# Kernel tuning notes

Measured on AMD Instinct MI355X. Metric: run time of the kernel, lower is better.

The kernel has to match this reference:

```python
import jax, jax.numpy as jnp
import numpy as np

N = 100000      # nodes
E = 1600000     # directed edges (avg degree 16)
IN, HID, OUT = 128, 128, 64


def setup_inputs() -> dict:
    key = jax.random.key(0)
    ks = jax.random.split(key, 6)
    x = jax.random.normal(ks[0], (N, IN), dtype=jnp.float32)
    edge_index = jax.random.randint(ks[1], (2, E), 0, N, dtype=jnp.int32)
    W1 = jax.random.normal(ks[2], (IN, HID), dtype=jnp.float32) * (1.0 / np.sqrt(IN))
    b1 = jax.random.normal(ks[3], (HID,), dtype=jnp.float32) * 0.01
    W2 = jax.random.normal(ks[4], (HID, OUT), dtype=jnp.float32) * (1.0 / np.sqrt(HID))
    b2 = jax.random.normal(ks[5], (OUT,), dtype=jnp.float32) * 0.01
    return {"x": x, "edge_index": edge_index, "W1": W1, "b1": b1, "W2": W2, "b2": b2}


def _gcn_norm(edge_index):
    # add self-loops, compute symmetric normalization deg^-1/2 A_hat deg^-1/2
    loop = jnp.arange(N, dtype=edge_index.dtype)
    row = jnp.concatenate([edge_index[0], loop])  # source
    col = jnp.concatenate([edge_index[1], loop])  # target
    deg = jax.ops.segment_sum(jnp.ones(row.shape[0], jnp.float32), col, num_segments=N)
    dinv = jnp.where(deg > 0, jax.lax.rsqrt(deg), 0.0)
    norm = dinv[row] * dinv[col]  # [E+N]
    return row, col, norm


def _gcn_conv(x, row, col, norm, W, b):
    h = x @ W                              # [N, out] dense transform first (fewer features moved)
    msg = h[row] * norm[:, None]           # gather over edges
    agg = jax.ops.segment_sum(msg, col, num_segments=N)  # scatter-add to targets
    return agg + b


def reference(x, edge_index, W1, b1, W2, b2):
    row, col, norm = _gcn_norm(edge_index)
    h = jax.nn.relu(_gcn_conv(x, row, col, norm, W1, b1))
    return _gcn_conv(h, row, col, norm, W2, b2)
```

## Files before the change

### kernel.cpp

```cpp
#include <hip/hip_runtime.h>

#define NN 100000
#define NE 1600000

#define BSH 9
#define BSZ 512
#define NBUK 196
#define CAP 12288
#define CHUNK 4096
#define EPT 16

typedef _Float16 hs8 __attribute__((ext_vector_type(8)));
typedef float f32x4 __attribute__((ext_vector_type(4)));
typedef float f32x2 __attribute__((ext_vector_type(2)));
#define MFMA16H(a, b, c) __builtin_amdgcn_mfma_f32_16x16x32_f16(a, b, c, 0, 0, 0)

static inline size_t alignup(size_t x) { return (x + 255) & ~(size_t)255; }

union h8u { uint4 q; _Float16 h[8]; };


__global__ __launch_bounds__(256) void k_prep0(int* __restrict__ gcur,
                                               const float* __restrict__ W1, _Float16* __restrict__ WT1,
                                               const float* __restrict__ W2, _Float16* __restrict__ WT2) {
  int b = blockIdx.x, t = threadIdx.x;
  if (b < 64) {
    int i = b * 256 + t;
    int k = i >> 7, c = i & 127;
    WT1[c * 128 + k] = (_Float16)W1[i];
  } else if (b < 96) {
    int i = (b - 64) * 256 + t;
    int k = i >> 6, c = i & 63;
    WT2[c * 128 + k] = (_Float16)W2[i];
  } else {
    if (t < NBUK) gcur[t] = t * CAP;
  }
}

__global__ __launch_bounds__(256) void k_bucket(const int* __restrict__ row, const int* __restrict__ col,
                                                int* __restrict__ gcur, uint* __restrict__ pr_pack) {
  __shared__ int cnt[NBUK];
  int t = threadIdx.x;
  for (int i = t; i < NBUK; i += 256) cnt[i] = 0;
  __syncthreads();
  int e0 = blockIdx.x * CHUNK;
  int rr[EPT], cc[EPT];
#pragma unroll
  for (int i = 0; i < EPT; i++) {
    int e = e0 + t + i * 256;
    bool ok = e < NE;
    cc[i] = ok ? col[e] : -1;
    rr[i] = ok ? row[e] : 0;
  }
#pragma unroll
  for (int i = 0; i < EPT; i++)
    if (cc[i] >= 0) atomicAdd(&cnt[cc[i] >> BSH], 1);
  __syncthreads();
  for (int i = t; i < NBUK; i += 256) {
    int c = cnt[i];
    cnt[i] = c ? atomicAdd(&gcur[i], c) : 0;
  }
  __syncthreads();
#pragma unroll
  for (int i = 0; i < EPT; i++)
    if (cc[i] >= 0) {
      int p = atomicAdd(&cnt[cc[i] >> BSH], 1);
      pr_pack[p] = ((uint)rr[i] << BSH) | (uint)(cc[i] & (BSZ - 1));
    }
}

__global__ __launch_bounds__(256) void k_bdeg(const uint* __restrict__ pr_pack, const int* __restrict__ gcur,
                                              int* __restrict__ deg, float* __restrict__ dinv,
                                              int* __restrict__ bsums) {
  __shared__ int dc[BSZ];
  int t = threadIdx.x, b = blockIdx.x;
  for (int i = t; i < BSZ; i += 256) dc[i] = 0;
  __syncthreads();
  int s = b * CAP;
  int n = min(gcur[b] - s, CAP);
  for (int i = t; i < n; i += 256) atomicAdd(&dc[pr_pack[s + i] & (BSZ - 1)], 1);
  __syncthreads();
  int nb0 = b << BSH;
  for (int i = t; i < BSZ; i += 256) {
    int node = nb0 + i;
    if (node < NN) {
      int d = dc[i] + 1;
      deg[node] = d;
      dinv[node] = rsqrtf((float)d);
    }
  }
  if (t == 0) bsums[b] = n + min(BSZ, NN - nb0);
}

__global__ __launch_bounds__(256) void k_scanB(int* __restrict__ bsums) {
  __shared__ int sm[256];
  int t = threadIdx.x;
  int v = (t < NBUK) ? bsums[t] : 0;
  sm[t] = v;
  __syncthreads();
  for (int d = 1; d < 256; d <<= 1) {
    int tmp = (t >= d) ? sm[t - d] : 0;
    __syncthreads();
    sm[t] += tmp;
    __syncthreads();
  }
  if (t < NBUK) bsums[t] = sm[t] - v;
}

__global__ __launch_bounds__(256) void k_bfill(const uint* __restrict__ pr_pack, const int* __restrict__ gcur,
                                               const int* __restrict__ deg, const float* __restrict__ dinv,
                                               const int* __restrict__ bsums, int* __restrict__ offs,
                                               uint2* __restrict__ wcsr) {
  __shared__ int loff[BSZ];
  __shared__ int cur[BSZ];
  __shared__ float dl[BSZ];
  __shared__ int tsum[256];
  int t = threadIdx.x, b = blockIdx.x;
  int nb0 = b << BSH;
  int i0 = 2 * t, i1 = i0 + 1;
  int n0 = nb0 + i0, n1 = nb0 + i1;
  int d0 = (n0 < NN) ? deg[n0] : 0;
  int d1 = (n1 < NN) ? deg[n1] : 0;
  int v = d0 + d1;
  tsum[t] = v;
  __syncthreads();
  for (int d = 1; d < 256; d <<= 1) {
    int tmp = (t >= d) ? tsum[t - d] : 0;
    __syncthreads();
    tsum[t] += tmp;
    __syncthreads();
  }
  int base = bsums[b] + tsum[t] - v;
  float dv0 = (n0 < NN) ? dinv[n0] : 0.f;
  float dv1 = (n1 < NN) ? dinv[n1] : 0.f;
  loff[i0] = base;
  loff[i1] = base + d0;
  dl[i0] = dv0;
  dl[i1] = dv1;
  cur[i0] = 1;
  cur[i1] = 1;
  if (n0 < NN) {
    offs[n0] = base;
    wcsr[base] = make_uint2((uint)n0, __float_as_uint(dv0 * dv0));
  }
  if (n1 < NN) {
    offs[n1] = base + d0;
    wcsr[base + d0] = make_uint2((uint)n1, __float_as_uint(dv1 * dv1));
  }
  __syncthreads();
  int s = b * CAP;
  int n = min(gcur[b] - s, CAP);
  for (int i = t; i < n; i += 256) {
    uint prk = pr_pack[s + i];
    int li = (int)(prk & (BSZ - 1));
    uint r = prk >> BSH;
    int p = atomicAdd(&cur[li], 1);
    wcsr[loff[li] + p] = make_uint2(r, __float_as_uint(dinv[r] * dl[li]));
  }
}


__global__ __launch_bounds__(256) void k_gemm128(const float* __restrict__ x, const _Float16* __restrict__ WT,
                                                 unsigned char* __restrict__ t8) {
  int wave = threadIdx.x >> 6, lane = threadIdx.x & 63;
  int col0 = wave * 32;
  int lr = lane & 15;
  int lk = (lane >> 4) * 8;
  hs8 bfrag[2][4];
#pragma unroll
  for (int n = 0; n < 2; n++)
#pragma unroll
    for (int ks = 0; ks < 4; ks++)
      bfrag[n][ks] = *(const hs8*)&WT[(size_t)(col0 + n * 16 + lr) * 128 + ks * 32 + lk];
  int row0 = blockIdx.x * 64;
#pragma unroll 1
  for (int mt = 0; mt < 4; mt++) {
    int r0 = row0 + mt * 16;
    if (r0 >= NN) return;
    const float* xr = x + (size_t)(r0 + lr) * 128 + lk;
    f32x4 acc[2] = {{0.f, 0.f, 0.f, 0.f}, {0.f, 0.f, 0.f, 0.f}};
#pragma unroll
    for (int ks = 0; ks < 4; ks++) {
      float4 a0 = *(const float4*)&xr[ks * 32];
      float4 a1 = *(const float4*)&xr[ks * 32 + 4];
      hs8 af;
      af[0] = (_Float16)a0.x; af[1] = (_Float16)a0.y;
      af[2] = (_Float16)a0.z; af[3] = (_Float16)a0.w;
      af[4] = (_Float16)a1.x; af[5] = (_Float16)a1.y;
      af[6] = (_Float16)a1.z; af[7] = (_Float16)a1.w;
      acc[0] = MFMA16H(af, bfrag[0][ks], acc[0]);
      acc[1] = MFMA16H(af, bfrag[1][ks], acc[1]);
    }
    int rbase = r0 + (lane >> 4) * 4;
#pragma unroll
    for (int n = 0; n < 2; n++)
#pragma unroll
      for (int r = 0; r < 4; r++) {
        uint e = (uint)__builtin_amdgcn_cvt_pk_fp8_f32(acc[n][r], acc[n][r], 0, false);
        t8[(size_t)(rbase + r) * 128 + col0 + n * 16 + lr] = (unsigned char)(e & 0xffu);
      }
  }
}

__global__ __launch_bounds__(256) void k_gemm64(const _Float16* __restrict__ h, const _Float16* __restrict__ WT,
                                                _Float16* __restrict__ t2) {
  int wave = threadIdx.x >> 6, lane = threadIdx.x & 63;
  int col0 = wave * 16;
  int lr = lane & 15;
  int lk = (lane >> 4) * 8;
  hs8 bfrag[4];
#pragma unroll
  for (int ks = 0; ks < 4; ks++)
    bfrag[ks] = *(const hs8*)&WT[(size_t)(col0 + lr) * 128 + ks * 32 + lk];
  int row0 = blockIdx.x * 64;
#pragma unroll 1
  for (int mt = 0; mt < 4; mt++) {
    int r0 = row0 + mt * 16;
    if (r0 >= NN) return;
    const _Float16* hr = h + (size_t)(r0 + lr) * 128 + lk;
    f32x4 acc = {0.f, 0.f, 0.f, 0.f};
#pragma unroll
    for (int ks = 0; ks < 4; ks++) {
      hs8 af = *(const hs8*)&hr[ks * 32];
      acc = MFMA16H(af, bfrag[ks], acc);
    }
    int rbase = r0 + (lane >> 4) * 4;
#pragma unroll
    for (int r = 0; r < 4; r++)
      t2[(size_t)(rbase + r) * 64 + col0 + lr] = (_Float16)acc[r];
  }
}


__global__ __launch_bounds__(256) void k_agg128(const unsigned char* __restrict__ t8, const int* __restrict__ offs,
                                                const int* __restrict__ deg, const uint2* __restrict__ wcsr,
                                                const float* __restrict__ bias, _Float16* __restrict__ out) {
  int wave = threadIdx.x >> 6, lane = threadIdx.x & 63;
  int half = lane >> 5;
  int sub = (lane >> 4) & 1;
  int f = lane & 15;
  int node = blockIdx.x * 8 + wave * 2 + half;
  int beg = offs[node];
  int d = deg[node];
  const char* tb = (const char*)t8;
  float acc[8] = {};
  int trips = (d + 1) >> 1;
  uint2 e = (sub < d) ? wcsr[beg + sub] : make_uint2(0u, 0u);
#pragma unroll 1
  for (int k = 0; k < trips; k++) {
    int ns = (k + 1) * 2 + sub;
    uint2 en = (ns < d) ? wcsr[beg + ns] : make_uint2(0u, 0u);
    float s = __uint_as_float(e.y);
    uint2 u = *(const uint2*)(tb + (((size_t)e.x) << 7) + (f << 3));
    f32x2 p0 = __builtin_amdgcn_cvt_pk_f32_fp8(u.x, false);
    f32x2 p1 = __builtin_amdgcn_cvt_pk_f32_fp8(u.x, true);
    f32x2 p2 = __builtin_amdgcn_cvt_pk_f32_fp8(u.y, false);
    f32x2 p3 = __builtin_amdgcn_cvt_pk_f32_fp8(u.y, true);
    acc[0] = fmaf(p0[0], s, acc[0]);
    acc[1] = fmaf(p0[1], s, acc[1]);
    acc[2] = fmaf(p1[0], s, acc[2]);
    acc[3] = fmaf(p1[1], s, acc[3]);
    acc[4] = fmaf(p2[0], s, acc[4]);
    acc[5] = fmaf(p2[1], s, acc[5]);
    acc[6] = fmaf(p3[0], s, acc[6]);
    acc[7] = fmaf(p3[1], s, acc[7]);
    e = en;
  }
#pragma unroll
  for (int j = 0; j < 8; j++) acc[j] += __shfl_xor(acc[j], 16);
  if (sub == 0) {
    float4 b0 = *(const float4*)&bias[f * 8];
    float4 b1 = *(const float4*)&bias[f * 8 + 4];
    h8u st;
    st.h[0] = (_Float16)fmaxf(acc[0] + b0.x, 0.f);
    st.h[1] = (_Float16)fmaxf(acc[1] + b0.y, 0.f);
    st.h[2] = (_Float16)fmaxf(acc[2] + b0.z, 0.f);
    st.h[3] = (_Float16)fmaxf(acc[3] + b0.w, 0.f);
    st.h[4] = (_Float16)fmaxf(acc[4] + b1.x, 0.f);
    st.h[5] = (_Float16)fmaxf(acc[5] + b1.y, 0.f);
    st.h[6] = (_Float16)fmaxf(acc[6] + b1.z, 0.f);
    st.h[7] = (_Float16)fmaxf(acc[7] + b1.w, 0.f);
    *(uint4*)&out[(size_t)node * 128 + f * 8] = st.q;
  }
}

__global__ __launch_bounds__(256) void k_agg64(const _Float16* __restrict__ t, const int* __restrict__ offs,
                                               const int* __restrict__ deg, const uint2* __restrict__ wcsr,
                                               const float* __restrict__ bias, float* __restrict__ out) {
  int wave = threadIdx.x >> 6, lane = threadIdx.x & 63;
  int half = lane >> 5;
  int sub = (lane >> 3) & 3;
  int f8 = lane & 7;
  int node = blockIdx.x * 8 + wave * 2 + half;
  int beg = offs[node];
  int d = deg[node];
  const char* tb = (const char*)t;
  float acc[8] = {};
  int trips = (d + 3) >> 2;
  uint2 e = (sub < d) ? wcsr[beg + sub] : make_uint2(0u, 0u);
#pragma unroll 1
  for (int k = 0; k < trips; k++) {
    int ns = (k + 1) * 4 + sub;
    uint2 en = (ns < d) ? wcsr[beg + ns] : make_uint2(0u, 0u);
    float s = __uint_as_float(e.y);
    h8u u;
    u.q = *(const uint4*)(tb + (((size_t)e.x) << 7) + (f8 << 4));
    acc[0] = fmaf((float)u.h[0], s, acc[0]);
    acc[1] = fmaf((float)u.h[1], s, acc[1]);
    acc[2] = fmaf((float)u.h[2], s, acc[2]);
    acc[3] = fmaf((float)u.h[3], s, acc[3]);
    acc[4] = fmaf((float)u.h[4], s, acc[4]);
    acc[5] = fmaf((float)u.h[5], s, acc[5]);
    acc[6] = fmaf((float)u.h[6], s, acc[6]);
    acc[7] = fmaf((float)u.h[7], s, acc[7]);
    e = en;
  }
#pragma unroll
  for (int j = 0; j < 8; j++) {
    acc[j] += __shfl_xor(acc[j], 8);
    acc[j] += __shfl_xor(acc[j], 16);
  }
  if (sub == 0) {
    float4 b0 = *(const float4*)&bias[f8 * 8];
    float4 b1 = *(const float4*)&bias[f8 * 8 + 4];
    float4 o0 = make_float4(acc[0] + b0.x, acc[1] + b0.y, acc[2] + b0.z, acc[3] + b0.w);
    float4 o1 = make_float4(acc[4] + b1.x, acc[5] + b1.y, acc[6] + b1.z, acc[7] + b1.w);
    *(float4*)&out[(size_t)node * 64 + f8 * 8] = o0;
    *(float4*)&out[(size_t)node * 64 + f8 * 8 + 4] = o1;
  }
}


extern "C" void kernel_launch(void* const* d_in, const int* in_sizes, int n_in,
                              void* d_out, int out_size, void* d_ws, size_t ws_size,
                              hipStream_t stream) {
  const float* x  = (const float*)d_in[0];
  const int*   ei = (const int*)d_in[1];
  const float* W1 = (const float*)d_in[2];
  const float* b1 = (const float*)d_in[3];
  const float* W2 = (const float*)d_in[4];
  const float* b2 = (const float*)d_in[5];
  float* out = (float*)d_out;

  char* p = (char*)d_ws;
  int* deg       = (int*)p;      p += alignup((size_t)NN * 4);
  int* gcur      = (int*)p;      p += alignup((size_t)NBUK * 4);
  int* offs      = (int*)p;      p += alignup((size_t)NN * 4);
  int* bsums     = (int*)p;      p += alignup(256 * 4);
  float* dinv    = (float*)p;    p += alignup((size_t)NN * 4);
  uint2* wcsr    = (uint2*)p;    p += alignup((size_t)(NE + NN + 64) * 8);
  _Float16* WT1  = (_Float16*)p; p += alignup(128 * 128 * 2);
  _Float16* WT2  = (_Float16*)p; p += alignup(64 * 128 * 2);
  unsigned char* t8 = (unsigned char*)p; p += alignup((size_t)NN * 128);
  _Float16* t2   = (_Float16*)p; p += alignup((size_t)NN * 64 * 2);
  _Float16* h1   = (_Float16*)p; p += alignup((size_t)NN * 128 * 2);
  uint* pr_pack  = (uint*)t2;
  (void)ws_size; (void)in_sizes; (void)n_in; (void)out_size;

  const int* row = ei;
  const int* col = ei + NE;

  int nbB = (NE + CHUNK - 1) / CHUNK;

  k_prep0<<<97, 256, 0, stream>>>(gcur, W1, WT1, W2, WT2);
  k_bucket<<<nbB, 256, 0, stream>>>(row, col, gcur, pr_pack);
  k_bdeg<<<NBUK, 256, 0, stream>>>(pr_pack, gcur, deg, dinv, bsums);
  k_scanB<<<1, 256, 0, stream>>>(bsums);
  k_bfill<<<NBUK, 256, 0, stream>>>(pr_pack, gcur, deg, dinv, bsums, offs, wcsr);

  int nbG = (NN + 63) / 64;
  int nbA = NN / 8;
  k_gemm128<<<nbG, 256, 0, stream>>>(x, WT1, t8);
  k_agg128<<<nbA, 256, 0, stream>>>(t8, offs, deg, wcsr, b1, h1);
  k_gemm64<<<nbG, 256, 0, stream>>>(h1, WT2, t2);
  k_agg64<<<nbA, 256, 0, stream>>>(t2, offs, deg, wcsr, b2, out);
}
```

Baseline: 195.5 us.

## Fuse edge bucketing with first GEMM, drop scan kernel, software-pipeline aggregations

Edge bucketing and the first dense transform now run in one launch, with separate block ranges, so they can overlap on the device. The block-sum scan kernel is removed: each fill block reserves its CSR segment base with an atomic on a global counter. CSR segments therefore land in arbitrary block order, which is fine because aggregation reads them through offs and deg. Both aggregation kernels prefetch edge records two steps ahead and feature rows one step ahead to hide gather latency, and the 128-wide one uses packed two-wide FMAs. The cost is more live registers and one extra speculative gather per node.

```diff
diff --git a/kernel.cpp b/kernel.cpp
--- a/kernel.cpp
+++ b/kernel.cpp
@@ -20,7 +20,7 @@
 union h8u { uint4 q; _Float16 h[8]; };
 
 
-__global__ __launch_bounds__(256) void k_prep0(int* __restrict__ gcur,
+__global__ __launch_bounds__(256) void k_prep0(int* __restrict__ gcur, int* __restrict__ gtotal,
                                                const float* __restrict__ W1, _Float16* __restrict__ WT1,
                                                const float* __restrict__ W2, _Float16* __restrict__ WT2) {
   int b = blockIdx.x, t = threadIdx.x;
@@ -34,134 +34,13 @@
     WT2[c * 128 + k] = (_Float16)W2[i];
   } else {
     if (t < NBUK) gcur[t] = t * CAP;
-  }
-}
-
-__global__ __launch_bounds__(256) void k_bucket(const int* __restrict__ row, const int* __restrict__ col,
-                                                int* __restrict__ gcur, uint* __restrict__ pr_pack) {
-  __shared__ int cnt[NBUK];
-  int t = threadIdx.x;
-  for (int i = t; i < NBUK; i += 256) cnt[i] = 0;
-  __syncthreads();
-  int e0 = blockIdx.x * CHUNK;
-  int rr[EPT], cc[EPT];
-#pragma unroll
-  for (int i = 0; i < EPT; i++) {
-    int e = e0 + t + i * 256;
-    bool ok = e < NE;
-    cc[i] = ok ? col[e] : -1;
-    rr[i] = ok ? row[e] : 0;
-  }
-#pragma unroll
-  for (int i = 0; i < EPT; i++)
-    if (cc[i] >= 0) atomicAdd(&cnt[cc[i] >> BSH], 1);
-  __syncthreads();
-  for (int i = t; i < NBUK; i += 256) {
-    int c = cnt[i];
-    cnt[i] = c ? atomicAdd(&gcur[i], c) : 0;
-  }
-  __syncthreads();
-#pragma unroll
-  for (int i = 0; i < EPT; i++)
-    if (cc[i] >= 0) {
-      int p = atomicAdd(&cnt[cc[i] >> BSH], 1);
-      pr_pack[p] = ((uint)rr[i] << BSH) | (uint)(cc[i] & (BSZ - 1));
-    }
-}
-
-__global__ __launch_bounds__(256) void k_bdeg(const uint* __restrict__ pr_pack, const int* __restrict__ gcur,
-                                              int* __restrict__ deg, float* __restrict__ dinv,
-                                              int* __restrict__ bsums) {
-  __shared__ int dc[BSZ];
-  int t = threadIdx.x, b = blockIdx.x;
-  for (int i = t; i < BSZ; i += 256) dc[i] = 0;
-  __syncthreads();
-  int s = b * CAP;
-  int n = min(gcur[b] - s, CAP);
-  for (int i = t; i < n; i += 256) atomicAdd(&dc[pr_pack[s + i] & (BSZ - 1)], 1);
-  __syncthreads();
-  int nb0 = b << BSH;
-  for (int i = t; i < BSZ; i += 256) {
-    int node = nb0 + i;
-    if (node < NN) {
-      int d = dc[i] + 1;
-      deg[node] = d;
-      dinv[node] = rsqrtf((float)d);
-    }
-  }
-  if (t == 0) bsums[b] = n + min(BSZ, NN - nb0);
-}
-
-__global__ __launch_bounds__(256) void k_scanB(int* __restrict__ bsums) {
-  __shared__ int sm[256];
-  int t = threadIdx.x;
-  int v = (t < NBUK) ? bsums[t] : 0;
-  sm[t] = v;
-  __syncthreads();
-  for (int d = 1; d < 256; d <<= 1) {
-    int tmp = (t >= d) ? sm[t - d] : 0;
-    __syncthreads();
-    sm[t] += tmp;
-    __syncthreads();
-  }
-  if (t < NBUK) bsums[t] = sm[t] - v;
-}
-
-__global__ __launch_bounds__(256) void k_bfill(const uint* __restrict__ pr_pack, const int* __restrict__ gcur,
-                                               const int* __restrict__ deg, const float* __restrict__ dinv,
-                                               const int* __restrict__ bsums, int* __restrict__ offs,
-                                               uint2* __restrict__ wcsr) {
-  __shared__ int loff[BSZ];
-  __shared__ int cur[BSZ];
-  __shared__ float dl[BSZ];
-  __shared__ int tsum[256];
-  int t = threadIdx.x, b = blockIdx.x;
-  int nb0 = b << BSH;
-  int i0 = 2 * t, i1 = i0 + 1;
-  int n0 = nb0 + i0, n1 = nb0 + i1;
-  int d0 = (n0 < NN) ? deg[n0] : 0;
-  int d1 = (n1 < NN) ? deg[n1] : 0;
-  int v = d0 + d1;
-  tsum[t] = v;
-  __syncthreads();
-  for (int d = 1; d < 256; d <<= 1) {
-    int tmp = (t >= d) ? tsum[t - d] : 0;
-    __syncthreads();
-    tsum[t] += tmp;
-    __syncthreads();
-  }
-  int base = bsums[b] + tsum[t] - v;
-  float dv0 = (n0 < NN) ? dinv[n0] : 0.f;
-  float dv1 = (n1 < NN) ? dinv[n1] : 0.f;
-  loff[i0] = base;
-  loff[i1] = base + d0;
-  dl[i0] = dv0;
-  dl[i1] = dv1;
-  cur[i0] = 1;
-  cur[i1] = 1;
-  if (n0 < NN) {
-    offs[n0] = base;
-    wcsr[base] = make_uint2((uint)n0, __float_as_uint(dv0 * dv0));
-  }
-  if (n1 < NN) {
-    offs[n1] = base + d0;
-    wcsr[base + d0] = make_uint2((uint)n1, __float_as_uint(dv1 * dv1));
-  }
-  __syncthreads();
-  int s = b * CAP;
-  int n = min(gcur[b] - s, CAP);
-  for (int i = t; i < n; i += 256) {
-    uint prk = pr_pack[s + i];
-    int li = (int)(prk & (BSZ - 1));
-    uint r = prk >> BSH;
-    int p = atomicAdd(&cur[li], 1);
-    wcsr[loff[li] + p] = make_uint2(r, __float_as_uint(dinv[r] * dl[li]));
-  }
-}
-
-
-__global__ __launch_bounds__(256) void k_gemm128(const float* __restrict__ x, const _Float16* __restrict__ WT,
-                                                 unsigned char* __restrict__ t8) {
+    if (t == 0) *gtotal = 0;
+  }
+}
+
+
+__device__ __forceinline__ void gemm128_body(const float* __restrict__ x, const _Float16* __restrict__ WT,
+                                             unsigned char* __restrict__ t8, int bid) {
   int wave = threadIdx.x >> 6, lane = threadIdx.x & 63;
   int col0 = wave * 32;
   int lr = lane & 15;
@@ -172,7 +51,7 @@
 #pragma unroll
     for (int ks = 0; ks < 4; ks++)
       bfrag[n][ks] = *(const hs8*)&WT[(size_t)(col0 + n * 16 + lr) * 128 + ks * 32 + lk];
-  int row0 = blockIdx.x * 64;
+  int row0 = bid * 64;
 #pragma unroll 1
   for (int mt = 0; mt < 4; mt++) {
     int r0 = row0 + mt * 16;
@@ -202,6 +81,124 @@
   }
 }
 
+
+__global__ __launch_bounds__(256) void k_fused1(const int* __restrict__ row, const int* __restrict__ col,
+                                                int* __restrict__ gcur, uint* __restrict__ pr_pack,
+                                                const float* __restrict__ x, const _Float16* __restrict__ WT,
+                                                unsigned char* __restrict__ t8, int nbB) {
+  if ((int)blockIdx.x >= nbB) {
+    gemm128_body(x, WT, t8, (int)blockIdx.x - nbB);
+    return;
+  }
+  __shared__ int cnt[NBUK];
+  int t = threadIdx.x;
+  for (int i = t; i < NBUK; i += 256) cnt[i] = 0;
+  __syncthreads();
+  int e0 = blockIdx.x * CHUNK;
+  int rr[EPT], cc[EPT];
+#pragma unroll
+  for (int i = 0; i < EPT; i++) {
+    int e = e0 + t + i * 256;
+    bool ok = e < NE;
+    cc[i] = ok ? col[e] : -1;
+    rr[i] = ok ? row[e] : 0;
+  }
+#pragma unroll
+  for (int i = 0; i < EPT; i++)
+    if (cc[i] >= 0) atomicAdd(&cnt[cc[i] >> BSH], 1);
+  __syncthreads();
+  for (int i = t; i < NBUK; i += 256) {
+    int c = cnt[i];
+    cnt[i] = c ? atomicAdd(&gcur[i], c) : 0;
+  }
+  __syncthreads();
+#pragma unroll
+  for (int i = 0; i < EPT; i++)
+    if (cc[i] >= 0) {
+      int p = atomicAdd(&cnt[cc[i] >> BSH], 1);
+      pr_pack[p] = ((uint)rr[i] << BSH) | (uint)(cc[i] & (BSZ - 1));
+    }
+}
+
+
+__global__ __launch_bounds__(256) void k_bdeg(const uint* __restrict__ pr_pack, const int* __restrict__ gcur,
+                                              int* __restrict__ deg, float* __restrict__ dinv) {
+  __shared__ int dc[BSZ];
+  int t = threadIdx.x, b = blockIdx.x;
+  for (int i = t; i < BSZ; i += 256) dc[i] = 0;
+  __syncthreads();
+  int s = b * CAP;
+  int n = min(gcur[b] - s, CAP);
+  for (int i = t; i < n; i += 256) atomicAdd(&dc[pr_pack[s + i] & (BSZ - 1)], 1);
+  __syncthreads();
+  int nb0 = b << BSH;
+  for (int i = t; i < BSZ; i += 256) {
+    int node = nb0 + i;
+    if (node < NN) {
+      int d = dc[i] + 1;
+      deg[node] = d;
+      dinv[node] = rsqrtf((float)d);
+    }
+  }
+}
+
+
+__global__ __launch_bounds__(256) void k_bfill(const uint* __restrict__ pr_pack, const int* __restrict__ gcur,
+                                               const int* __restrict__ deg, const float* __restrict__ dinv,
+                                               int* __restrict__ gtotal, int* __restrict__ offs,
+                                               uint2* __restrict__ wcsr) {
+  __shared__ int loff[BSZ];
+  __shared__ int cur[BSZ];
+  __shared__ float dl[BSZ];
+  __shared__ int tsum[256];
+  __shared__ int sbase;
+  int t = threadIdx.x, b = blockIdx.x;
+  int nb0 = b << BSH;
+  int i0 = 2 * t, i1 = i0 + 1;
+  int n0 = nb0 + i0, n1 = nb0 + i1;
+  int d0 = (n0 < NN) ? deg[n0] : 0;
+  int d1 = (n1 < NN) ? deg[n1] : 0;
+  int v = d0 + d1;
+  tsum[t] = v;
+  __syncthreads();
+  for (int d = 1; d < 256; d <<= 1) {
+    int tmp = (t >= d) ? tsum[t - d] : 0;
+    __syncthreads();
+    tsum[t] += tmp;
+    __syncthreads();
+  }
+  if (t == 255) sbase = atomicAdd(gtotal, tsum[255]);
+  __syncthreads();
+  int base = sbase + tsum[t] - v;
+  float dv0 = (n0 < NN) ? dinv[n0] : 0.f;
+  float dv1 = (n1 < NN) ? dinv[n1] : 0.f;
+  loff[i0] = base;
+  loff[i1] = base + d0;
+  dl[i0] = dv0;
+  dl[i1] = dv1;
+  cur[i0] = 1;
+  cur[i1] = 1;
+  if (n0 < NN) {
+    offs[n0] = base;
+    wcsr[base] = make_uint2((uint)n0, __float_as_uint(dv0 * dv0));
+  }
+  if (n1 < NN) {
+    offs[n1] = base + d0;
+    wcsr[base + d0] = make_uint2((uint)n1, __float_as_uint(dv1 * dv1));
+  }
+  __syncthreads();
+  int s = b * CAP;
+  int n = min(gcur[b] - s, CAP);
+  for (int i = t; i < n; i += 256) {
+    uint prk = pr_pack[s + i];
+    int li = (int)(prk & (BSZ - 1));
+    uint r = prk >> BSH;
+    int p = atomicAdd(&cur[li], 1);
+    wcsr[loff[li] + p] = make_uint2(r, __float_as_uint(dinv[r] * dl[li]));
+  }
+}
+
+
 __global__ __launch_bounds__(256) void k_gemm64(const _Float16* __restrict__ h, const _Float16* __restrict__ WT,
                                                 _Float16* __restrict__ t2) {
   int wave = threadIdx.x >> 6, lane = threadIdx.x & 63;
@@ -243,43 +240,46 @@
   int beg = offs[node];
   int d = deg[node];
   const char* tb = (const char*)t8;
-  float acc[8] = {};
+  f32x2 acc2[4] = {};
   int trips = (d + 1) >> 1;
-  uint2 e = (sub < d) ? wcsr[beg + sub] : make_uint2(0u, 0u);
+  uint2 e0 = (sub < d) ? wcsr[beg + sub] : make_uint2(0u, 0u);
+  int ns = 2 + sub;
+  uint2 e1 = (ns < d) ? wcsr[beg + ns] : make_uint2(0u, 0u);
+  uint2 u0 = *(const uint2*)(tb + (((size_t)e0.x) << 7) + (f << 3));
 #pragma unroll 1
   for (int k = 0; k < trips; k++) {
-    int ns = (k + 1) * 2 + sub;
-    uint2 en = (ns < d) ? wcsr[beg + ns] : make_uint2(0u, 0u);
-    float s = __uint_as_float(e.y);
-    uint2 u = *(const uint2*)(tb + (((size_t)e.x) << 7) + (f << 3));
-    f32x2 p0 = __builtin_amdgcn_cvt_pk_f32_fp8(u.x, false);
-    f32x2 p1 = __builtin_amdgcn_cvt_pk_f32_fp8(u.x, true);
-    f32x2 p2 = __builtin_amdgcn_cvt_pk_f32_fp8(u.y, false);
-    f32x2 p3 = __builtin_amdgcn_cvt_pk_f32_fp8(u.y, true);
-    acc[0] = fmaf(p0[0], s, acc[0]);
-    acc[1] = fmaf(p0[1], s, acc[1]);
-    acc[2] = fmaf(p1[0], s, acc[2]);
-    acc[3] = fmaf(p1[1], s, acc[3]);
-    acc[4] = fmaf(p2[0], s, acc[4]);
-    acc[5] = fmaf(p2[1], s, acc[5]);
-    acc[6] = fmaf(p3[0], s, acc[6]);
-    acc[7] = fmaf(p3[1], s, acc[7]);
-    e = en;
-  }
-#pragma unroll
-  for (int j = 0; j < 8; j++) acc[j] += __shfl_xor(acc[j], 16);
+    int n2 = (k + 2) * 2 + sub;
+    uint2 e2 = (n2 < d) ? wcsr[beg + n2] : make_uint2(0u, 0u);
+    uint2 u1 = *(const uint2*)(tb + (((size_t)e1.x) << 7) + (f << 3));
+    float s = __uint_as_float(e0.y);
+    f32x2 s2 = {s, s};
+    f32x2 p0 = __builtin_amdgcn_cvt_pk_f32_fp8(u0.x, false);
+    f32x2 p1 = __builtin_amdgcn_cvt_pk_f32_fp8(u0.x, true);
+    f32x2 p2 = __builtin_amdgcn_cvt_pk_f32_fp8(u0.y, false);
+    f32x2 p3 = __builtin_amdgcn_cvt_pk_f32_fp8(u0.y, true);
+    acc2[0] = __builtin_elementwise_fma(p0, s2, acc2[0]);
+    acc2[1] = __builtin_elementwise_fma(p1, s2, acc2[1]);
+    acc2[2] = __builtin_elementwise_fma(p2, s2, acc2[2]);
+    acc2[3] = __builtin_elementwise_fma(p3, s2, acc2[3]);
+    e0 = e1; e1 = e2; u0 = u1;
+  }
+  float a[8];
+#pragma unroll
+  for (int j = 0; j < 4; j++) { a[2 * j] = acc2[j][0]; a[2 * j + 1] = acc2[j][1]; }
+#pragma unroll
+  for (int j = 0; j < 8; j++) a[j] += __shfl_xor(a[j], 16);
   if (sub == 0) {
     float4 b0 = *(const float4*)&bias[f * 8];
     float4 b1 = *(const float4*)&bias[f * 8 + 4];
     h8u st;
-    st.h[0] = (_Float16)fmaxf(acc[0] + b0.x, 0.f);
-    st.h[1] = (_Float16)fmaxf(acc[1] + b0.y, 0.f);
-    st.h[2] = (_Float16)fmaxf(acc[2] + b0.z, 0.f);
-    st.h[3] = (_Float16)fmaxf(acc[3] + b0.w, 0.f);
-    st.h[4] = (_Float16)fmaxf(acc[4] + b1.x, 0.f);
-    st.h[5] = (_Float16)fmaxf(acc[5] + b1.y, 0.f);
-    st.h[6] = (_Float16)fmaxf(acc[6] + b1.z, 0.f);
-    st.h[7] = (_Float16)fmaxf(acc[7] + b1.w, 0.f);
+    st.h[0] = (_Float16)fmaxf(a[0] + b0.x, 0.f);
+    st.h[1] = (_Float16)fmaxf(a[1] + b0.y, 0.f);
+    st.h[2] = (_Float16)fmaxf(a[2] + b0.z, 0.f);
+    st.h[3] = (_Float16)fmaxf(a[3] + b0.w, 0.f);
+    st.h[4] = (_Float16)fmaxf(a[4] + b1.x, 0.f);
+    st.h[5] = (_Float16)fmaxf(a[5] + b1.y, 0.f);
+    st.h[6] = (_Float16)fmaxf(a[6] + b1.z, 0.f);
+    st.h[7] = (_Float16)fmaxf(a[7] + b1.w, 0.f);
     *(uint4*)&out[(size_t)node * 128 + f * 8] = st.q;
   }
 }
@@ -297,23 +297,27 @@
   const char* tb = (const char*)t;
   float acc[8] = {};
   int trips = (d + 3) >> 2;
-  uint2 e = (sub < d) ? wcsr[beg + sub] : make_uint2(0u, 0u);
+  uint2 e0 = (sub < d) ? wcsr[beg + sub] : make_uint2(0u, 0u);
+  int ns = 4 + sub;
+  uint2 e1 = (ns < d) ? wcsr[beg + ns] : make_uint2(0u, 0u);
+  h8u u0;
+  u0.q = *(const uint4*)(tb + (((size_t)e0.x) << 7) + (f8 << 4));
 #pragma unroll 1
   for (int k = 0; k < trips; k++) {
-    int ns = (k + 1) * 4 + sub;
-    uint2 en = (ns < d) ? wcsr[beg + ns] : make_uint2(0u, 0u);
-    float s = __uint_as_float(e.y);
-    h8u u;
-    u.q = *(const uint4*)(tb + (((size_t)e.x) << 7) + (f8 << 4));
-    acc[0] = fmaf((float)u.h[0], s, acc[0]);
-    acc[1] = fmaf((float)u.h[1], s, acc[1]);
-    acc[2] = fmaf((float)u.h[2], s, acc[2]);
-    acc[3] = fmaf((float)u.h[3], s, acc[3]);
-    acc[4] = fmaf((float)u.h[4], s, acc[4]);
-    acc[5] = fmaf((float)u.h[5], s, acc[5]);
-    acc[6] = fmaf((float)u.h[6], s, acc[6]);
-    acc[7] = fmaf((float)u.h[7], s, acc[7]);
-    e = en;
+    int n2 = (k + 2) * 4 + sub;
+    uint2 e2 = (n2 < d) ? wcsr[beg + n2] : make_uint2(0u, 0u);
+    h8u u1;
+    u1.q = *(const uint4*)(tb + (((size_t)e1.x) << 7) + (f8 << 4));
+    float s = __uint_as_float(e0.y);
+    acc[0] = fmaf((float)u0.h[0], s, acc[0]);
+    acc[1] = fmaf((float)u0.h[1], s, acc[1]);
+    acc[2] = fmaf((float)u0.h[2], s, acc[2]);
+    acc[3] = fmaf((float)u0.h[3], s, acc[3]);
+    acc[4] = fmaf((float)u0.h[4], s, acc[4]);
+    acc[5] = fmaf((float)u0.h[5], s, acc[5]);
+    acc[6] = fmaf((float)u0.h[6], s, acc[6]);
+    acc[7] = fmaf((float)u0.h[7], s, acc[7]);
+    e0 = e1; e1 = e2; u0 = u1;
   }
 #pragma unroll
   for (int j = 0; j < 8; j++) {
@@ -346,7 +350,7 @@
   int* deg       = (int*)p;      p += alignup((size_t)NN * 4);
   int* gcur      = (int*)p;      p += alignup((size_t)NBUK * 4);
   int* offs      = (int*)p;      p += alignup((size_t)NN * 4);
-  int* bsums     = (int*)p;      p += alignup(256 * 4);
+  int* gtotal    = (int*)p;      p += alignup(256);
   float* dinv    = (float*)p;    p += alignup((size_t)NN * 4);
   uint2* wcsr    = (uint2*)p;    p += alignup((size_t)(NE + NN + 64) * 8);
   _Float16* WT1  = (_Float16*)p; p += alignup(128 * 128 * 2);
@@ -361,16 +365,13 @@
   const int* col = ei + NE;
 
   int nbB = (NE + CHUNK - 1) / CHUNK;
-
-  k_prep0<<<97, 256, 0, stream>>>(gcur, W1, WT1, W2, WT2);
-  k_bucket<<<nbB, 256, 0, stream>>>(row, col, gcur, pr_pack);
-  k_bdeg<<<NBUK, 256, 0, stream>>>(pr_pack, gcur, deg, dinv, bsums);
-  k_scanB<<<1, 256, 0, stream>>>(bsums);
-  k_bfill<<<NBUK, 256, 0, stream>>>(pr_pack, gcur, deg, dinv, bsums, offs, wcsr);
-
   int nbG = (NN + 63) / 64;
   int nbA = NN / 8;
-  k_gemm128<<<nbG, 256, 0, stream>>>(x, WT1, t8);
+
+  k_prep0<<<97, 256, 0, stream>>>(gcur, gtotal, W1, WT1, W2, WT2);
+  k_fused1<<<nbB + nbG, 256, 0, stream>>>(row, col, gcur, pr_pack, x, WT1, t8, nbB);
+  k_bdeg<<<NBUK, 256, 0, stream>>>(pr_pack, gcur, deg, dinv);
+  k_bfill<<<NBUK, 256, 0, stream>>>(pr_pack, gcur, deg, dinv, gtotal, offs, wcsr);
   k_agg128<<<nbA, 256, 0, stream>>>(t8, offs, deg, wcsr, b1, h1);
   k_gemm64<<<nbG, 256, 0, stream>>>(h1, WT2, t2);
   k_agg64<<<nbA, 256, 0, stream>>>(t2, offs, deg, wcsr, b2, out);
```

Measured after the change: 183.5 us. 6.1% less time.

## Fuse edge bucketing with first GEMM and merge CSR build kernels

Applied to the files above, without the earlier changes.

The edge bucketing pass and the first dense transform now run as one horizontally fused launch, so the two independent workloads can overlap. Degree counting, the bucket-offset scan and the CSR fill are merged into one kernel. It uses a grid-wide atomic barrier to publish dinv, then an atomic ticket for bucket base offsets, and keeps bucket edges in LDS so they are not reread. In-block ranks are packed into the row bits so the second shared atomic pass is gone. This cuts four launches, but relies on all 196 blocks being co-resident for the spin barrier, and the atomic ticket makes the CSR order nondeterministic across buckets.

```diff
diff --git a/kernel.cpp b/kernel.cpp
--- a/kernel.cpp
+++ b/kernel.cpp
@@ -20,7 +20,7 @@
 union h8u { uint4 q; _Float16 h[8]; };
 
 
-__global__ __launch_bounds__(256) void k_prep0(int* __restrict__ gcur,
+__global__ __launch_bounds__(256) void k_prep0(int* __restrict__ gcur, int* __restrict__ gctl,
                                                const float* __restrict__ W1, _Float16* __restrict__ WT1,
                                                const float* __restrict__ W2, _Float16* __restrict__ WT2) {
   int b = blockIdx.x, t = threadIdx.x;
@@ -34,134 +34,13 @@
     WT2[c * 128 + k] = (_Float16)W2[i];
   } else {
     if (t < NBUK) gcur[t] = t * CAP;
-  }
-}
-
-__global__ __launch_bounds__(256) void k_bucket(const int* __restrict__ row, const int* __restrict__ col,
-                                                int* __restrict__ gcur, uint* __restrict__ pr_pack) {
-  __shared__ int cnt[NBUK];
-  int t = threadIdx.x;
-  for (int i = t; i < NBUK; i += 256) cnt[i] = 0;
-  __syncthreads();
-  int e0 = blockIdx.x * CHUNK;
-  int rr[EPT], cc[EPT];
-#pragma unroll
-  for (int i = 0; i < EPT; i++) {
-    int e = e0 + t + i * 256;
-    bool ok = e < NE;
-    cc[i] = ok ? col[e] : -1;
-    rr[i] = ok ? row[e] : 0;
-  }
-#pragma unroll
-  for (int i = 0; i < EPT; i++)
-    if (cc[i] >= 0) atomicAdd(&cnt[cc[i] >> BSH], 1);
-  __syncthreads();
-  for (int i = t; i < NBUK; i += 256) {
-    int c = cnt[i];
-    cnt[i] = c ? atomicAdd(&gcur[i], c) : 0;
-  }
-  __syncthreads();
-#pragma unroll
-  for (int i = 0; i < EPT; i++)
-    if (cc[i] >= 0) {
-      int p = atomicAdd(&cnt[cc[i] >> BSH], 1);
-      pr_pack[p] = ((uint)rr[i] << BSH) | (uint)(cc[i] & (BSZ - 1));
-    }
-}
-
-__global__ __launch_bounds__(256) void k_bdeg(const uint* __restrict__ pr_pack, const int* __restrict__ gcur,
-                                              int* __restrict__ deg, float* __restrict__ dinv,
-                                              int* __restrict__ bsums) {
-  __shared__ int dc[BSZ];
-  int t = threadIdx.x, b = blockIdx.x;
-  for (int i = t; i < BSZ; i += 256) dc[i] = 0;
-  __syncthreads();
-  int s = b * CAP;
-  int n = min(gcur[b] - s, CAP);
-  for (int i = t; i < n; i += 256) atomicAdd(&dc[pr_pack[s + i] & (BSZ - 1)], 1);
-  __syncthreads();
-  int nb0 = b << BSH;
-  for (int i = t; i < BSZ; i += 256) {
-    int node = nb0 + i;
-    if (node < NN) {
-      int d = dc[i] + 1;
-      deg[node] = d;
-      dinv[node] = rsqrtf((float)d);
-    }
-  }
-  if (t == 0) bsums[b] = n + min(BSZ, NN - nb0);
-}
-
-__global__ __launch_bounds__(256) void k_scanB(int* __restrict__ bsums) {
-  __shared__ int sm[256];
-  int t = threadIdx.x;
-  int v = (t < NBUK) ? bsums[t] : 0;
-  sm[t] = v;
-  __syncthreads();
-  for (int d = 1; d < 256; d <<= 1) {
-    int tmp = (t >= d) ? sm[t - d] : 0;
-    __syncthreads();
-    sm[t] += tmp;
-    __syncthreads();
-  }
-  if (t < NBUK) bsums[t] = sm[t] - v;
-}
-
-__global__ __launch_bounds__(256) void k_bfill(const uint* __restrict__ pr_pack, const int* __restrict__ gcur,
-                                               const int* __restrict__ deg, const float* __restrict__ dinv,
-                                               const int* __restrict__ bsums, int* __restrict__ offs,
-                                               uint2* __restrict__ wcsr) {
-  __shared__ int loff[BSZ];
-  __shared__ int cur[BSZ];
-  __shared__ float dl[BSZ];
-  __shared__ int tsum[256];
-  int t = threadIdx.x, b = blockIdx.x;
-  int nb0 = b << BSH;
-  int i0 = 2 * t, i1 = i0 + 1;
-  int n0 = nb0 + i0, n1 = nb0 + i1;
-  int d0 = (n0 < NN) ? deg[n0] : 0;
-  int d1 = (n1 < NN) ? deg[n1] : 0;
-  int v = d0 + d1;
-  tsum[t] = v;
-  __syncthreads();
-  for (int d = 1; d < 256; d <<= 1) {
-    int tmp = (t >= d) ? tsum[t - d] : 0;
-    __syncthreads();
-    tsum[t] += tmp;
-    __syncthreads();
-  }
-  int base = bsums[b] + tsum[t] - v;
-  float dv0 = (n0 < NN) ? dinv[n0] : 0.f;
-  float dv1 = (n1 < NN) ? dinv[n1] : 0.f;
-  loff[i0] = base;
-  loff[i1] = base + d0;
-  dl[i0] = dv0;
-  dl[i1] = dv1;
-  cur[i0] = 1;
-  cur[i1] = 1;
-  if (n0 < NN) {
-    offs[n0] = base;
-    wcsr[base] = make_uint2((uint)n0, __float_as_uint(dv0 * dv0));
-  }
-  if (n1 < NN) {
-    offs[n1] = base + d0;
-    wcsr[base + d0] = make_uint2((uint)n1, __float_as_uint(dv1 * dv1));
-  }
-  __syncthreads();
-  int s = b * CAP;
-  int n = min(gcur[b] - s, CAP);
-  for (int i = t; i < n; i += 256) {
-    uint prk = pr_pack[s + i];
-    int li = (int)(prk & (BSZ - 1));
-    uint r = prk >> BSH;
-    int p = atomicAdd(&cur[li], 1);
-    wcsr[loff[li] + p] = make_uint2(r, __float_as_uint(dinv[r] * dl[li]));
-  }
-}
-
-
-__global__ __launch_bounds__(256) void k_gemm128(const float* __restrict__ x, const _Float16* __restrict__ WT,
-                                                 unsigned char* __restrict__ t8) {
+    if (t == 0) { gctl[0] = 0; gctl[16] = 0; }
+  }
+}
+
+
+__device__ __forceinline__ void gemm128_body(const float* __restrict__ x, const _Float16* __restrict__ WT,
+                                             unsigned char* __restrict__ t8, int bid) {
   int wave = threadIdx.x >> 6, lane = threadIdx.x & 63;
   int col0 = wave * 32;
   int lr = lane & 15;
@@ -172,7 +51,7 @@
 #pragma unroll
     for (int ks = 0; ks < 4; ks++)
       bfrag[n][ks] = *(const hs8*)&WT[(size_t)(col0 + n * 16 + lr) * 128 + ks * 32 + lk];
-  int row0 = blockIdx.x * 64;
+  int row0 = bid * 64;
 #pragma unroll 1
   for (int mt = 0; mt < 4; mt++) {
     int r0 = row0 + mt * 16;
@@ -201,6 +80,132 @@
       }
   }
 }
+
+
+__global__ __launch_bounds__(256) void k_fused1(const int* __restrict__ row, const int* __restrict__ col,
+                                                int* __restrict__ gcur, uint* __restrict__ pr_pack,
+                                                const float* __restrict__ x, const _Float16* __restrict__ WT,
+                                                unsigned char* __restrict__ t8, int nbB) {
+  if ((int)blockIdx.x >= nbB) {
+    gemm128_body(x, WT, t8, (int)blockIdx.x - nbB);
+    return;
+  }
+  __shared__ int cnt[NBUK];
+  int t = threadIdx.x;
+  for (int i = t; i < NBUK; i += 256) cnt[i] = 0;
+  __syncthreads();
+  int e0 = blockIdx.x * CHUNK;
+  uint rr[EPT]; int cc[EPT];
+#pragma unroll
+  for (int i = 0; i < EPT; i++) {
+    int e = e0 + t + i * 256;
+    bool ok = e < NE;
+    cc[i] = ok ? col[e] : -1;
+    rr[i] = ok ? (uint)row[e] : 0u;
+  }
+#pragma unroll
+  for (int i = 0; i < EPT; i++)
+    if (cc[i] >= 0) {
+      uint rank = (uint)atomicAdd(&cnt[cc[i] >> BSH], 1);
+      rr[i] |= rank << 17;
+    }
+  __syncthreads();
+  for (int i = t; i < NBUK; i += 256) {
+    int c = cnt[i];
+    cnt[i] = c ? atomicAdd(&gcur[i], c) : 0;
+  }
+  __syncthreads();
+#pragma unroll
+  for (int i = 0; i < EPT; i++)
+    if (cc[i] >= 0) {
+      int p = cnt[cc[i] >> BSH] + (int)(rr[i] >> 17);
+      pr_pack[p] = ((rr[i] & 0x1FFFFu) << BSH) | (uint)(cc[i] & (BSZ - 1));
+    }
+}
+
+
+__global__ __launch_bounds__(256) void k_build(const uint* __restrict__ pr_pack, const int* __restrict__ gcur,
+                                               int* __restrict__ deg, float* __restrict__ dinv,
+                                               int* __restrict__ gctl, int* __restrict__ offs,
+                                               uint2* __restrict__ wcsr) {
+  __shared__ uint ep[CAP];
+  __shared__ int dc[BSZ];
+  __shared__ float dl[BSZ];
+  __shared__ int loff[BSZ];
+  __shared__ int cur[BSZ];
+  __shared__ int tsum[256];
+  __shared__ int sbase;
+  int t = threadIdx.x, b = blockIdx.x;
+  for (int i = t; i < BSZ; i += 256) dc[i] = 0;
+  __syncthreads();
+  int s = b * CAP;
+  int n = min(gcur[b] - s, CAP);
+  for (int i = t; i < n; i += 256) {
+    uint v = pr_pack[s + i];
+    ep[i] = v;
+    atomicAdd(&dc[v & (BSZ - 1)], 1);
+  }
+  __syncthreads();
+  int nb0 = b << BSH;
+  for (int i = t; i < BSZ; i += 256) {
+    int node = nb0 + i;
+    if (node < NN) {
+      int d = dc[i] + 1;
+      deg[node] = d;
+      float dv = rsqrtf((float)d);
+      dinv[node] = dv;
+      dl[i] = dv;
+    } else {
+      dl[i] = 0.f;
+    }
+  }
+  __threadfence();
+  __syncthreads();
+  if (t == 0) {
+    __hip_atomic_fetch_add(&gctl[16], 1, __ATOMIC_ACQ_REL, __HIP_MEMORY_SCOPE_AGENT);
+    while (__hip_atomic_load(&gctl[16], __ATOMIC_ACQUIRE, __HIP_MEMORY_SCOPE_AGENT) < NBUK) {}
+  }
+  __syncthreads();
+  __threadfence();
+  int i0 = 2 * t, i1 = i0 + 1;
+  int n0 = nb0 + i0, n1 = nb0 + i1;
+  int d0 = (n0 < NN) ? dc[i0] + 1 : 0;
+  int d1 = (n1 < NN) ? dc[i1] + 1 : 0;
+  int v = d0 + d1;
+  tsum[t] = v;
+  __syncthreads();
+  for (int d = 1; d < 256; d <<= 1) {
+    int tmp = (t >= d) ? tsum[t - d] : 0;
+    __syncthreads();
+    tsum[t] += tmp;
+    __syncthreads();
+  }
+  if (t == 255) sbase = atomicAdd(&gctl[0], tsum[255]);
+  __syncthreads();
+  int base = sbase + tsum[t] - v;
+  loff[i0] = base;
+  loff[i1] = base + d0;
+  cur[i0] = 1;
+  cur[i1] = 1;
+  if (n0 < NN) {
+    offs[n0] = base;
+    wcsr[base] = make_uint2((uint)n0, __float_as_uint(dl[i0] * dl[i0]));
+  }
+  if (n1 < NN) {
+    offs[n1] = base + d0;
+    wcsr[base + d0] = make_uint2((uint)n1, __float_as_uint(dl[i1] * dl[i1]));
+  }
+  __syncthreads();
+  for (int i = t; i < n; i += 256) {
+    uint prk = ep[i];
+    int li = (int)(prk & (BSZ - 1));
+    uint r = prk >> BSH;
+    int p = atomicAdd(&cur[li], 1);
+    uint dru = __hip_atomic_load((const uint*)&dinv[r], __ATOMIC_RELAXED, __HIP_MEMORY_SCOPE_AGENT);
+    wcsr[loff[li] + p] = make_uint2(r, __float_as_uint(__uint_as_float(dru) * dl[li]));
+  }
+}
+
 
 __global__ __launch_bounds__(256) void k_gemm64(const _Float16* __restrict__ h, const _Float16* __restrict__ WT,
                                                 _Float16* __restrict__ t2) {
@@ -346,7 +351,7 @@
   int* deg       = (int*)p;      p += alignup((size_t)NN * 4);
   int* gcur      = (int*)p;      p += alignup((size_t)NBUK * 4);
   int* offs      = (int*)p;      p += alignup((size_t)NN * 4);
-  int* bsums     = (int*)p;      p += alignup(256 * 4);
+  int* gctl      = (int*)p;      p += alignup(256);
   float* dinv    = (float*)p;    p += alignup((size_t)NN * 4);
   uint2* wcsr    = (uint2*)p;    p += alignup((size_t)(NE + NN + 64) * 8);
   _Float16* WT1  = (_Float16*)p; p += alignup(128 * 128 * 2);
@@ -361,16 +366,12 @@
   const int* col = ei + NE;
 
   int nbB = (NE + CHUNK - 1) / CHUNK;
-
-  k_prep0<<<97, 256, 0, stream>>>(gcur, W1, WT1, W2, WT2);
-  k_bucket<<<nbB, 256, 0, stream>>>(row, col, gcur, pr_pack);
-  k_bdeg<<<NBUK, 256, 0, stream>>>(pr_pack, gcur, deg, dinv, bsums);
-  k_scanB<<<1, 256, 0, stream>>>(bsums);
-  k_bfill<<<NBUK, 256, 0, stream>>>(pr_pack, gcur, deg, dinv, bsums, offs, wcsr);
-
   int nbG = (NN + 63) / 64;
   int nbA = NN / 8;
-  k_gemm128<<<nbG, 256, 0, stream>>>(x, WT1, t8);
+
+  k_prep0<<<97, 256, 0, stream>>>(gcur, gctl, W1, WT1, W2, WT2);
+  k_fused1<<<nbB + nbG, 256, 0, stream>>>(row, col, gcur, pr_pack, x, WT1, t8, nbB);
+  k_build<<<NBUK, 256, 0, stream>>>(pr_pack, gcur, deg, dinv, gctl, offs, wcsr);
   k_agg128<<<nbA, 256, 0, stream>>>(t8, offs, deg, wcsr, b1, h1);
   k_gemm64<<<nbG, 256, 0, stream>>>(h1, WT2, t2);
   k_agg64<<<nbA, 256, 0, stream>>>(t2, offs, deg, wcsr, b2, out);
```

Result: slower. 208.5 us (+6.7%).

## Fuse preprocessing launches, reuse atomic ranks, replace block scan with atomic offsets

Applied to the files above, without the earlier changes.

The weight transpose moves into extra blocks of the bucketing kernel, and the degree-count kernel shares one launch with the first GEMM. The single-block scan kernel is removed: each fill block claims its CSR base with an atomicAdd on a global counter. The bucketing pass keeps the rank returned by its first shared atomic, packed into the upper row bits, so the second round of shared atomics is no longer needed. The aim is fewer launches and serialization points, plus overlap of GEMM work with degree counting, at the cost of a CSR segment order that depends on scheduling rather than being deterministic.

```diff
diff --git a/kernel.cpp b/kernel.cpp
--- a/kernel.cpp
+++ b/kernel.cpp
@@ -20,64 +20,115 @@
 union h8u { uint4 q; _Float16 h[8]; };
 
 
-__global__ __launch_bounds__(256) void k_prep0(int* __restrict__ gcur,
-                                               const float* __restrict__ W1, _Float16* __restrict__ WT1,
-                                               const float* __restrict__ W2, _Float16* __restrict__ WT2) {
-  int b = blockIdx.x, t = threadIdx.x;
-  if (b < 64) {
-    int i = b * 256 + t;
-    int k = i >> 7, c = i & 127;
-    WT1[c * 128 + k] = (_Float16)W1[i];
-  } else if (b < 96) {
-    int i = (b - 64) * 256 + t;
-    int k = i >> 6, c = i & 63;
-    WT2[c * 128 + k] = (_Float16)W2[i];
-  } else {
-    if (t < NBUK) gcur[t] = t * CAP;
-  }
-}
-
 __global__ __launch_bounds__(256) void k_bucket(const int* __restrict__ row, const int* __restrict__ col,
-                                                int* __restrict__ gcur, uint* __restrict__ pr_pack) {
+                                                int* __restrict__ gcur, uint* __restrict__ pr_pack,
+                                                const float* __restrict__ W1, _Float16* __restrict__ WT1,
+                                                const float* __restrict__ W2, _Float16* __restrict__ WT2,
+                                                int nbB) {
+  int b = (int)blockIdx.x, t = threadIdx.x;
+  if (b >= nbB) {
+    int w = b - nbB;
+    if (w < 64) {
+      int i = w * 256 + t;
+      int k = i >> 7, c = i & 127;
+      WT1[c * 128 + k] = (_Float16)W1[i];
+    } else {
+      int i = (w - 64) * 256 + t;
+      int k = i >> 6, c = i & 63;
+      WT2[c * 128 + k] = (_Float16)W2[i];
+    }
+    return;
+  }
   __shared__ int cnt[NBUK];
-  int t = threadIdx.x;
   for (int i = t; i < NBUK; i += 256) cnt[i] = 0;
   __syncthreads();
-  int e0 = blockIdx.x * CHUNK;
-  int rr[EPT], cc[EPT];
+  int e0 = b * CHUNK;
+  uint rr[EPT]; int cc[EPT];
 #pragma unroll
   for (int i = 0; i < EPT; i++) {
     int e = e0 + t + i * 256;
     bool ok = e < NE;
     cc[i] = ok ? col[e] : -1;
-    rr[i] = ok ? row[e] : 0;
+    rr[i] = ok ? (uint)row[e] : 0u;
   }
 #pragma unroll
   for (int i = 0; i < EPT; i++)
-    if (cc[i] >= 0) atomicAdd(&cnt[cc[i] >> BSH], 1);
+    if (cc[i] >= 0) {
+      uint rank = (uint)atomicAdd(&cnt[cc[i] >> BSH], 1);
+      rr[i] |= rank << 17;
+    }
   __syncthreads();
   for (int i = t; i < NBUK; i += 256) {
     int c = cnt[i];
-    cnt[i] = c ? atomicAdd(&gcur[i], c) : 0;
+    cnt[i] = c ? (i * CAP + atomicAdd(&gcur[i], c)) : 0;
   }
   __syncthreads();
 #pragma unroll
   for (int i = 0; i < EPT; i++)
     if (cc[i] >= 0) {
-      int p = atomicAdd(&cnt[cc[i] >> BSH], 1);
-      pr_pack[p] = ((uint)rr[i] << BSH) | (uint)(cc[i] & (BSZ - 1));
-    }
-}
-
-__global__ __launch_bounds__(256) void k_bdeg(const uint* __restrict__ pr_pack, const int* __restrict__ gcur,
-                                              int* __restrict__ deg, float* __restrict__ dinv,
-                                              int* __restrict__ bsums) {
+      int p = cnt[cc[i] >> BSH] + (int)(rr[i] >> 17);
+      pr_pack[p] = ((rr[i] & 0x1FFFFu) << BSH) | (uint)(cc[i] & (BSZ - 1));
+    }
+}
+
+
+__device__ __forceinline__ void gemm128_body(const float* __restrict__ x, const _Float16* __restrict__ WT,
+                                             unsigned char* __restrict__ t8, int bid) {
+  int wave = threadIdx.x >> 6, lane = threadIdx.x & 63;
+  int col0 = wave * 32;
+  int lr = lane & 15;
+  int lk = (lane >> 4) * 8;
+  hs8 bfrag[2][4];
+#pragma unroll
+  for (int n = 0; n < 2; n++)
+#pragma unroll
+    for (int ks = 0; ks < 4; ks++)
+      bfrag[n][ks] = *(const hs8*)&WT[(size_t)(col0 + n * 16 + lr) * 128 + ks * 32 + lk];
+  int row0 = bid * 64;
+#pragma unroll 1
+  for (int mt = 0; mt < 4; mt++) {
+    int r0 = row0 + mt * 16;
+    if (r0 >= NN) return;
+    const float* xr = x + (size_t)(r0 + lr) * 128 + lk;
+    f32x4 acc[2] = {{0.f, 0.f, 0.f, 0.f}, {0.f, 0.f, 0.f, 0.f}};
+#pragma unroll
+    for (int ks = 0; ks < 4; ks++) {
+      float4 a0 = *(const float4*)&xr[ks * 32];
+      float4 a1 = *(const float4*)&xr[ks * 32 + 4];
+      hs8 af;
+      af[0] = (_Float16)a0.x; af[1] = (_Float16)a0.y;
+      af[2] = (_Float16)a0.z; af[3] = (_Float16)a0.w;
+      af[4] = (_Float16)a1.x; af[5] = (_Float16)a1.y;
+      af[6] = (_Float16)a1.z; af[7] = (_Float16)a1.w;
+      acc[0] = MFMA16H(af, bfrag[0][ks], acc[0]);
+      acc[1] = MFMA16H(af, bfrag[1][ks], acc[1]);
+    }
+    int rbase = r0 + (lane >> 4) * 4;
+#pragma unroll
+    for (int n = 0; n < 2; n++)
+#pragma unroll
+      for (int r = 0; r < 4; r++) {
+        uint e = (uint)__builtin_amdgcn_cvt_pk_fp8_f32(acc[n][r], acc[n][r], 0, false);
+        t8[(size_t)(rbase + r) * 128 + col0 + n * 16 + lr] = (unsigned char)(e & 0xffu);
+      }
+  }
+}
+
+
+__global__ __launch_bounds__(256) void k_fbg(const uint* __restrict__ pr_pack, const int* __restrict__ gcur,
+                                             int* __restrict__ deg, float* __restrict__ dinv,
+                                             const float* __restrict__ x, const _Float16* __restrict__ WT,
+                                             unsigned char* __restrict__ t8) {
+  if ((int)blockIdx.x >= NBUK) {
+    gemm128_body(x, WT, t8, (int)blockIdx.x - NBUK);
+    return;
+  }
   __shared__ int dc[BSZ];
   int t = threadIdx.x, b = blockIdx.x;
   for (int i = t; i < BSZ; i += 256) dc[i] = 0;
   __syncthreads();
   int s = b * CAP;
-  int n = min(gcur[b] - s, CAP);
+  int n = min(gcur[b], CAP);
   for (int i = t; i < n; i += 256) atomicAdd(&dc[pr_pack[s + i] & (BSZ - 1)], 1);
   __syncthreads();
   int nb0 = b << BSH;
@@ -89,32 +140,18 @@
       dinv[node] = rsqrtf((float)d);
     }
   }
-  if (t == 0) bsums[b] = n + min(BSZ, NN - nb0);
-}
-
-__global__ __launch_bounds__(256) void k_scanB(int* __restrict__ bsums) {
-  __shared__ int sm[256];
-  int t = threadIdx.x;
-  int v = (t < NBUK) ? bsums[t] : 0;
-  sm[t] = v;
-  __syncthreads();
-  for (int d = 1; d < 256; d <<= 1) {
-    int tmp = (t >= d) ? sm[t - d] : 0;
-    __syncthreads();
-    sm[t] += tmp;
-    __syncthreads();
-  }
-  if (t < NBUK) bsums[t] = sm[t] - v;
-}
+}
+
 
 __global__ __launch_bounds__(256) void k_bfill(const uint* __restrict__ pr_pack, const int* __restrict__ gcur,
                                                const int* __restrict__ deg, const float* __restrict__ dinv,
-                                               const int* __restrict__ bsums, int* __restrict__ offs,
+                                               int* __restrict__ gctl, int* __restrict__ offs,
                                                uint2* __restrict__ wcsr) {
   __shared__ int loff[BSZ];
   __shared__ int cur[BSZ];
   __shared__ float dl[BSZ];
   __shared__ int tsum[256];
+  __shared__ int sbase;
   int t = threadIdx.x, b = blockIdx.x;
   int nb0 = b << BSH;
   int i0 = 2 * t, i1 = i0 + 1;
@@ -130,7 +167,9 @@
     tsum[t] += tmp;
     __syncthreads();
   }
-  int base = bsums[b] + tsum[t] - v;
+  if (t == 255) sbase = atomicAdd(&gctl[0], tsum[255]);
+  __syncthreads();
+  int base = sbase + tsum[t] - v;
   float dv0 = (n0 < NN) ? dinv[n0] : 0.f;
   float dv1 = (n1 < NN) ? dinv[n1] : 0.f;
   loff[i0] = base;
@@ -149,7 +188,7 @@
   }
   __syncthreads();
   int s = b * CAP;
-  int n = min(gcur[b] - s, CAP);
+  int n = min(gcur[b], CAP);
   for (int i = t; i < n; i += 256) {
     uint prk = pr_pack[s + i];
     int li = (int)(prk & (BSZ - 1));
@@ -159,48 +198,6 @@
   }
 }
 
-
-__global__ __launch_bounds__(256) void k_gemm128(const float* __restrict__ x, const _Float16* __restrict__ WT,
-                                                 unsigned char* __restrict__ t8) {
-  int wave = threadIdx.x >> 6, lane = threadIdx.x & 63;
-  int col0 = wave * 32;
-  int lr = lane & 15;
-  int lk = (lane >> 4) * 8;
-  hs8 bfrag[2][4];
-#pragma unroll
-  for (int n = 0; n < 2; n++)
-#pragma unroll
-    for (int ks = 0; ks < 4; ks++)
-      bfrag[n][ks] = *(const hs8*)&WT[(size_t)(col0 + n * 16 + lr) * 128 + ks * 32 + lk];
-  int row0 = blockIdx.x * 64;
-#pragma unroll 1
-  for (int mt = 0; mt < 4; mt++) {
-    int r0 = row0 + mt * 16;
-    if (r0 >= NN) return;
-    const float* xr = x + (size_t)(r0 + lr) * 128 + lk;
-    f32x4 acc[2] = {{0.f, 0.f, 0.f, 0.f}, {0.f, 0.f, 0.f, 0.f}};
-#pragma unroll
-    for (int ks = 0; ks < 4; ks++) {
-      float4 a0 = *(const float4*)&xr[ks * 32];
-      float4 a1 = *(const float4*)&xr[ks * 32 + 4];
-      hs8 af;
-      af[0] = (_Float16)a0.x; af[1] = (_Float16)a0.y;
-      af[2] = (_Float16)a0.z; af[3] = (_Float16)a0.w;
-      af[4] = (_Float16)a1.x; af[5] = (_Float16)a1.y;
-      af[6] = (_Float16)a1.z; af[7] = (_Float16)a1.w;
-      acc[0] = MFMA16H(af, bfrag[0][ks], acc[0]);
-      acc[1] = MFMA16H(af, bfrag[1][ks], acc[1]);
-    }
-    int rbase = r0 + (lane >> 4) * 4;
-#pragma unroll
-    for (int n = 0; n < 2; n++)
-#pragma unroll
-      for (int r = 0; r < 4; r++) {
-        uint e = (uint)__builtin_amdgcn_cvt_pk_fp8_f32(acc[n][r], acc[n][r], 0, false);
-        t8[(size_t)(rbase + r) * 128 + col0 + n * 16 + lr] = (unsigned char)(e & 0xffu);
-      }
-  }
-}
 
 __global__ __launch_bounds__(256) void k_gemm64(const _Float16* __restrict__ h, const _Float16* __restrict__ WT,
                                                 _Float16* __restrict__ t2) {
@@ -343,10 +340,10 @@
   float* out = (float*)d_out;
 
   char* p = (char*)d_ws;
+  int* gcur      = (int*)p;      p += alignup((size_t)NBUK * 4);
+  int* gctl      = (int*)p;      p += alignup(256);
   int* deg       = (int*)p;      p += alignup((size_t)NN * 4);
-  int* gcur      = (int*)p;      p += alignup((size_t)NBUK * 4);
   int* offs      = (int*)p;      p += alignup((size_t)NN * 4);
-  int* bsums     = (int*)p;      p += alignup(256 * 4);
   float* dinv    = (float*)p;    p += alignup((size_t)NN * 4);
   uint2* wcsr    = (uint2*)p;    p += alignup((size_t)(NE + NN + 64) * 8);
   _Float16* WT1  = (_Float16*)p; p += alignup(128 * 128 * 2);
@@ -361,16 +358,13 @@
   const int* col = ei + NE;
 
   int nbB = (NE + CHUNK - 1) / CHUNK;
-
-  k_prep0<<<97, 256, 0, stream>>>(gcur, W1, WT1, W2, WT2);
-  k_bucket<<<nbB, 256, 0, stream>>>(row, col, gcur, pr_pack);
-  k_bdeg<<<NBUK, 256, 0, stream>>>(pr_pack, gcur, deg, dinv, bsums);
-  k_scanB<<<1, 256, 0, stream>>>(bsums);
-  k_bfill<<<NBUK, 256, 0, stream>>>(pr_pack, gcur, deg, dinv, bsums, offs, wcsr);
-
   int nbG = (NN + 63) / 64;
   int nbA = NN / 8;
-  k_gemm128<<<nbG, 256, 0, stream>>>(x, WT1, t8);
+
+  hipMemsetAsync(gcur, 0, alignup((size_t)NBUK * 4) + 256, stream);
+  k_bucket<<<nbB + 96, 256, 0, stream>>>(row, col, gcur, pr_pack, W1, WT1, W2, WT2, nbB);
+  k_fbg<<<NBUK + nbG, 256, 0, stream>>>(pr_pack, gcur, deg, dinv, x, WT1, t8);
+  k_bfill<<<NBUK, 256, 0, stream>>>(pr_pack, gcur, deg, dinv, gctl, offs, wcsr);
   k_agg128<<<nbA, 256, 0, stream>>>(t8, offs, deg, wcsr, b1, h1);
   k_gemm64<<<nbG, 256, 0, stream>>>(h1, WT2, t2);
   k_agg64<<<nbA, 256, 0, stream>>>(t2, offs, deg, wcsr, b2, out);
```

Result: faster. 185.2 us (-5.2%).
